# Optimization experiments

Hardware: AMD Instinct MI355X
Metric: run time of the kernel (lower is better)

The kernel has to match this reference:

```python
import jax, jax.numpy as jnp
import numpy as np

B, N, C = 8, 2000, 81
MAX_INST = 100
MIN_CONF = 0.7
NMS_THR = 0.3
BBOX_STD = jnp.array([0.1, 0.1, 0.2, 0.2], dtype=jnp.float32)
CLASS_OFFSET = 4.0  # per-class box offset so one NMS == per-class NMS


def setup_inputs() -> dict:
    key = jax.random.key(0)
    k1, k2, k3, k4 = jax.random.split(key, 4)
    # well-formed normalized rois: y1<y2, x1<x2
    ctr = jax.random.uniform(k1, (B, N, 2), minval=0.2, maxval=0.8)
    sz = jax.random.uniform(k2, (B, N, 2), minval=0.02, maxval=0.3)
    y1x1 = jnp.clip(ctr - 0.5 * sz, 0.0, 1.0)
    y2x2 = jnp.clip(ctr + 0.5 * sz, 0.0, 1.0)
    rois = jnp.concatenate([y1x1, y2x2], axis=-1).astype(jnp.float32)
    mrcnn_class = jax.nn.softmax(4.0 * jax.random.normal(k3, (B, N, C)), axis=-1).astype(jnp.float32)
    mrcnn_bbox = (0.1 * jax.random.normal(k4, (B, N, C, 4))).astype(jnp.float32)
    # meta: [image_id(1), orig_shape(3), image_shape(3), window(4), scale(1), active_class_ids(C)]
    meta_row = np.concatenate([
        np.array([0.0]), np.array([1024.0, 1024.0, 3.0]), np.array([1024.0, 1024.0, 3.0]),
        np.array([0.0, 0.0, 1024.0, 1024.0]), np.array([1.0]), np.ones(C)]).astype(np.float32)
    image_meta = jnp.broadcast_to(jnp.asarray(meta_row), (B, 12 + C))
    return {"rois": rois, "mrcnn_class": mrcnn_class, "mrcnn_bbox": mrcnn_bbox, "image_meta": image_meta}


def _apply_box_deltas(boxes, deltas):  # [N,4],[N,4]
    h = boxes[:, 2] - boxes[:, 0]
    w = boxes[:, 3] - boxes[:, 1]
    cy = boxes[:, 0] + 0.5 * h + deltas[:, 0] * h
    cx = boxes[:, 1] + 0.5 * w + deltas[:, 1] * w
    h = h * jnp.exp(deltas[:, 2])
    w = w * jnp.exp(deltas[:, 3])
    return jnp.stack([cy - 0.5 * h, cx - 0.5 * w, cy + 0.5 * h, cx + 0.5 * w], axis=1)


def _clip_boxes(boxes, window):  # window: [4]
    wy1, wx1, wy2, wx2 = window[0], window[1], window[2], window[3]
    y1 = jnp.clip(boxes[:, 0], wy1, wy2)
    x1 = jnp.clip(boxes[:, 1], wx1, wx2)
    y2 = jnp.clip(boxes[:, 2], wy1, wy2)
    x2 = jnp.clip(boxes[:, 3], wx1, wx2)
    return jnp.stack([y1, x1, y2, x2], axis=1)


def _pairwise_iou(b):  # [N,4] -> [N,N]
    area = (b[:, 2] - b[:, 0]) * (b[:, 3] - b[:, 1])
    iy = jnp.maximum(0.0, jnp.minimum(b[:, None, 2], b[None, :, 2]) - jnp.maximum(b[:, None, 0], b[None, :, 0]))
    ix = jnp.maximum(0.0, jnp.minimum(b[:, None, 3], b[None, :, 3]) - jnp.maximum(b[:, None, 1], b[None, :, 1]))
    inter = iy * ix
    return inter / (area[:, None] + area[None, :] - inter + 1e-12)


def _refine_one(rois, probs, deltas, window):
    n = rois.shape[0]
    class_ids = jnp.argmax(probs, axis=1)                      # [N]
    idx = jnp.arange(n)
    scores = probs[idx, class_ids]                              # [N]
    ds = deltas[idx, class_ids] * BBOX_STD                      # [N,4]
    refined = _clip_boxes(_apply_box_deltas(rois, ds), window)  # [N,4]
    valid = (class_ids > 0) & (scores >= MIN_CONF)
    # per-class NMS via class-offset trick (classes can never overlap)
    off_boxes = refined + CLASS_OFFSET * class_ids.astype(jnp.float32)[:, None]
    order = jnp.argsort(-jnp.where(valid, scores, -1.0))
    b_sorted = off_boxes[order]
    iou = _pairwise_iou(b_sorted)                               # [N,N]
    pos = jnp.arange(n)

    def body(keep, i):
        sup = keep[i] & (iou[i] > NMS_THR) & (pos > i)
        return keep & ~sup, None

    keep_sorted, _ = jax.lax.scan(body, valid[order], pos)
    keep = jnp.zeros(n, bool).at[order].set(keep_sorted)
    # per-class cap at MAX_INST (mirror max_output_size of per-class NMS)
    same = class_ids[:, None] == class_ids[None, :]
    before = (scores[None, :] > scores[:, None]) | ((scores[None, :] == scores[:, None]) & (pos[None, :] < pos[:, None]))
    rank = jnp.sum(keep[None, :] & same & before, axis=1)
    keep = keep & (rank < MAX_INST)
    # global top-k by score, pad with zeros
    masked = jnp.where(keep, scores, -1.0)
    top_scores, top_idx = jax.lax.top_k(masked, MAX_INST)
    valid_out = top_scores > 0.0
    det = jnp.concatenate([
        refined[top_idx],
        class_ids[top_idx].astype(jnp.float32)[:, None],
        scores[top_idx][:, None]], axis=1)                      # [MAX_INST,6]
    return jnp.where(valid_out[:, None], det, 0.0)


def reference(rois, mrcnn_class, mrcnn_bbox, image_meta):
    # normalize per-image window using image_shape of first image (as in original)
    image_shape = image_meta[0, 4:7]
    h, w = image_shape[0], image_shape[1]
    scale = jnp.stack([h, w, h, w]) - 1.0
    shift = jnp.array([0.0, 0.0, 1.0, 1.0], dtype=jnp.float32)
    window = (image_meta[:, 7:11] - shift) / scale              # [B,4]
    det = jax.vmap(_refine_one)(rois, mrcnn_class, mrcnn_bbox, window)
    return det.reshape(rois.shape[0], MAX_INST, 6)
```

## Files before the change

### kernel.cpp

```cpp
#include <hip/hip_runtime.h>
#include <stdint.h>

#define Bn 8
#define Nn 2000
#define Cc 81
#define META_STRIDE (12 + Cc)
#define MAXI 100
#define MINCONF 0.7f
#define NMSTHR 0.3f
#define PB_ROIS 128
#define PSTRIDE 83
#define SELT 320
#define SELCAP 512

__device__ __forceinline__ uint32_t ford(float f) {
    uint32_t u = __float_as_uint(f);
    return (u & 0x80000000u) ? ~u : (u | 0x80000000u);
}

__device__ __forceinline__ unsigned long long shflx64(unsigned long long v, int lx) {
    unsigned int lo = (unsigned int)v, hi = (unsigned int)(v >> 32);
    lo = (unsigned int)__shfl_xor((int)lo, lx, 64);
    hi = (unsigned int)__shfl_xor((int)hi, lx, 64);
    return ((unsigned long long)hi << 32) | lo;
}

__global__ void __launch_bounds__(256)
k_prep(const float* __restrict__ rois,
       const float* __restrict__ probs,
       const float* __restrict__ bbox,
       const float* __restrict__ meta,
       float* __restrict__ refined,
       float* __restrict__ score,
       int* __restrict__ cls,
       unsigned long long* __restrict__ keys) {
    __shared__ float sp[PB_ROIS * PSTRIDE];
    int tid  = threadIdx.x;
    int base = blockIdx.x * PB_ROIS;

    const float* gp = probs + (size_t)base * Cc;
    const int total = PB_ROIS * Cc;
    int r = tid / Cc, c = tid - r * Cc;
    for (int idx = tid; idx < total; idx += 256) {
        sp[r * PSTRIDE + c] = gp[idx];
        r += 3; c += 13;
        if (c >= Cc) { c -= Cc; r += 1; }
    }
    __syncthreads();

    int row  = tid >> 1;
    int half = tid & 1;
    const float* sr = sp + row * PSTRIDE;
    int   c0 = half ? 41 : 0;
    int   c1 = half ? Cc : 41;
    float v  = sr[c0];
    int   cb = c0;
    for (int cc2 = c0 + 1; cc2 < c1; ++cc2) {
        float x = sr[cc2];
        if (x > v) { v = x; cb = cc2; }
    }
    float vo = __shfl_xor(v, 1, 64);
    int   co = __shfl_xor(cb, 1, 64);
    float vA = half ? vo : v;   int cA = half ? co : cb;
    float vB = half ? v  : vo;  int cB = half ? cb : co;
    float sbest;  int cbest;
    if (vB > vA) { sbest = vB; cbest = cB; }
    else         { sbest = vA; cbest = cA; }

    if (half) return;
    int t = base + row;

    float4 d4 = reinterpret_cast<const float4*>(bbox)[(size_t)t * Cc + cbest];
    float dy = d4.x * 0.1f, dx = d4.y * 0.1f, dh = d4.z * 0.2f, dw = d4.w * 0.2f;

    float4 r4 = reinterpret_cast<const float4*>(rois)[t];
    float y1 = r4.x, x1 = r4.y, y2 = r4.z, x2 = r4.w;
    float h = y2 - y1, w = x2 - x1;
    float cy = y1 + 0.5f * h + dy * h;
    float cx = x1 + 0.5f * w + dx * w;
    h = h * expf(dh);
    w = w * expf(dw);
    float ny1 = cy - 0.5f * h, nx1 = cx - 0.5f * w;
    float ny2 = cy + 0.5f * h, nx2 = cx + 0.5f * w;

    int b = t / Nn;
    float sy = meta[4] - 1.0f, sx = meta[5] - 1.0f;
    const float* mb = meta + (size_t)b * META_STRIDE;
    float wy1 = mb[7] / sy;
    float wx1 = mb[8] / sx;
    float wy2 = (mb[9]  - 1.0f) / sy;
    float wx2 = (mb[10] - 1.0f) / sx;

    ny1 = fminf(fmaxf(ny1, wy1), wy2);
    nx1 = fminf(fmaxf(nx1, wx1), wx2);
    ny2 = fminf(fmaxf(ny2, wy1), wy2);
    nx2 = fminf(fmaxf(nx2, wx1), wx2);

    reinterpret_cast<float4*>(refined)[t] = float4{ny1, nx1, ny2, nx2};
    score[t] = sbest;
    cls[t]   = cbest;

    int i = t - b * Nn;
    bool valid = (cbest > 0) && (sbest >= MINCONF);
    float ks = valid ? sbest : -1.0f;
    keys[t] = ((unsigned long long)ford(ks) << 32) |
              (unsigned long long)(0xFFFFFFFFu - (uint32_t)i);
}

__global__ void __launch_bounds__(1024, 1)
k_nms(const unsigned long long* __restrict__ keys,
      const float* __restrict__ refined,
      const float* __restrict__ score,
      const int* __restrict__ cls,
      float* __restrict__ out) {
    __shared__ unsigned long long sk[SELCAP];
    __shared__ float4 sboxL[SELCAP];
    __shared__ int h1[256], h2[256], sc[257];
    __shared__ unsigned long long intraw[64];
    __shared__ unsigned long long extw[16];
    __shared__ int klist[128];
    __shared__ int sNk, sB, sSuf, sTheta, scnt;

    int b = blockIdx.x, tid = threadIdx.x;
    int wid = tid >> 6, lane = tid & 63;
    int e0 = tid << 1;

    const unsigned long long* kb = keys + (size_t)b * Nn;
    unsigned long long k0 = (e0     < Nn) ? kb[e0]     : 0ull;
    unsigned long long k1 = (e0 + 1 < Nn) ? kb[e0 + 1] : 0ull;

    if (tid < 256) { h1[tid] = 0; h2[tid] = 0; }
    if (tid < SELCAP) sk[tid] = 0ull;
    if (tid == 0) { sB = -2; sSuf = 0; sTheta = 0x8000; scnt = 0; sNk = 0; sc[256] = 0; }
    __syncthreads();

    if (k0 >> 63) atomicAdd(&h1[(int)(k0 >> 56) & 255], 1);
    if (k1 >> 63) atomicAdd(&h1[(int)(k1 >> 56) & 255], 1);
    __syncthreads();

    if (wid == 0) {
        int b0 = lane << 2;
        int v0 = h1[b0], v1 = h1[b0 + 1], v2 = h1[b0 + 2], v3 = h1[b0 + 3];
        int s3 = v3, s2 = v2 + s3, s1 = v1 + s2, s0 = v0 + s1;
        int G = s0;
        #pragma unroll
        for (int off = 1; off < 64; off <<= 1) {
            int u = __shfl_down(G, off, 64);
            if (lane + off < 64) G += u;
        }
        int A = G - s0;
        sc[b0] = A + s0; sc[b0 + 1] = A + s1; sc[b0 + 2] = A + s2; sc[b0 + 3] = A + s3;
    }
    __syncthreads();
    if (tid < 256) {
        int c = sc[tid], cn = sc[tid + 1];
        if (c >= SELT && cn < SELT) { sB = tid; sSuf = cn; }
    }
    __syncthreads();
    int B = sB;

    if (B >= 0) {
        if ((k0 >> 63) && (((int)(k0 >> 56) & 255) == B))
            atomicAdd(&h2[(int)(k0 >> 48) & 255], 1);
        if ((k1 >> 63) && (((int)(k1 >> 56) & 255) == B))
            atomicAdd(&h2[(int)(k1 >> 48) & 255], 1);
        __syncthreads();
        if (wid == 0) {
            int b0 = lane << 2;
            int v0 = h2[b0], v1 = h2[b0 + 1], v2 = h2[b0 + 2], v3 = h2[b0 + 3];
            int s3 = v3, s2 = v2 + s3, s1 = v1 + s2, s0 = v0 + s1;
            int G = s0;
            #pragma unroll
            for (int off = 1; off < 64; off <<= 1) {
                int u = __shfl_down(G, off, 64);
                if (lane + off < 64) G += u;
            }
            int A = G - s0;
            sc[b0] = A + s0; sc[b0 + 1] = A + s1; sc[b0 + 2] = A + s2; sc[b0 + 3] = A + s3;
        }
        __syncthreads();
        if (tid < 256) {
            int c  = sSuf + sc[tid];
            int cn = sSuf + sc[tid + 1];
            if (c >= SELT && cn < SELT) sTheta = (B << 8) | tid;
        }
    }
    __syncthreads();

    unsigned th = (unsigned)sTheta;
    if ((unsigned)(k0 >> 48) >= th) {
        int s = atomicAdd(&scnt, 1);
        if (s < SELCAP) sk[s] = k0;
    }
    if ((unsigned)(k1 >> 48) >= th) {
        int s = atomicAdd(&scnt, 1);
        if (s < SELCAP) sk[s] = k1;
    }
    __syncthreads();
    int S = scnt; if (S > SELCAP) S = SELCAP;

    if (tid < 256) {
        unsigned long long a = sk[e0], bv = sk[e0 + 1];
        for (int k = 2; k <= 128; k <<= 1) {
            bool desc = ((e0 & k) == 0);
            for (int j = k >> 1; j >= 2; j >>= 1) {
                int lx = j >> 1;
                bool keepmax = (desc == ((lane & lx) == 0));
                unsigned long long oa = shflx64(a, lx);
                unsigned long long ob = shflx64(bv, lx);
                a  = keepmax ? (a  > oa ? a  : oa) : (a  < oa ? a  : oa);
                bv = keepmax ? (bv > ob ? bv : ob) : (bv < ob ? bv : ob);
            }
            bool sw = desc ? (a < bv) : (a > bv);
            if (sw) { unsigned long long t2 = a; a = bv; bv = t2; }
        }
        sk[e0] = a; sk[e0 + 1] = bv;
    }
    __syncthreads();

    for (int k = 256; k <= SELCAP; k <<= 1) {
        for (int j = k >> 1; j >= 128; j >>= 1) {
            for (int t = tid; t < SELCAP; t += 1024) {
                int ixj = t ^ j;
                if (ixj > t) {
                    unsigned long long x = sk[t], y = sk[ixj];
                    bool desc = ((t & k) == 0);
                    if (desc ? (x < y) : (x > y)) { sk[t] = y; sk[ixj] = x; }
                }
            }
            __syncthreads();
        }
        if (tid < 256) {
            unsigned long long a = sk[e0], bv = sk[e0 + 1];
            bool desc = ((e0 & k) == 0);
            #pragma unroll
            for (int lx = 32; lx >= 1; lx >>= 1) {
                bool keepmax = (desc == ((lane & lx) == 0));
                unsigned long long oa = shflx64(a, lx);
                unsigned long long ob = shflx64(bv, lx);
                a  = keepmax ? (a  > oa ? a  : oa) : (a  < oa ? a  : oa);
                bv = keepmax ? (bv > ob ? bv : ob) : (bv < ob ? bv : ob);
            }
            bool sw = desc ? (a < bv) : (a > bv);
            if (sw) { unsigned long long t2 = a; a = bv; bv = t2; }
            sk[e0] = a; sk[e0 + 1] = bv;
        }
        __syncthreads();
    }

    for (int t = tid; t < S; t += 1024) {
        uint32_t oi = 0xFFFFFFFFu - (uint32_t)(sk[t] & 0xFFFFFFFFull);
        int gi = b * Nn + (int)oi;
        float off = 4.0f * (float)cls[gi];
        float4 rf = reinterpret_cast<const float4*>(refined)[gi];
        sboxL[t] = float4{rf.x + off, rf.y + off, rf.z + off, rf.w + off};
    }
    __syncthreads();

    int nblocks = (S + 63) >> 6;
    for (int t = 0; t < nblocks; ++t) {
        int base = t << 6;
        int nb = S - base; if (nb > 64) nb = 64;
        int K = sNk;

        float4 cb = (lane < nb) ? sboxL[base + lane] : float4{0.f, 0.f, 0.f, 0.f};
        float a2 = (cb.z - cb.x) * (cb.w - cb.y);

        bool supext = false;
        for (int k = wid; k < K; k += 16) {
            float4 kbx = sboxL[klist[k]];
            float ar = (kbx.z - kbx.x) * (kbx.w - kbx.y);
            float iy = fmaxf(0.0f, fminf(kbx.z, cb.z) - fmaxf(kbx.x, cb.x));
            float ix = fmaxf(0.0f, fminf(kbx.w, cb.w) - fmaxf(kbx.y, cb.y));
            float inter = iy * ix;
            float iou = inter / (ar + a2 - inter + 1e-12f);
            supext |= (lane < nb) && (iou > NMSTHR);
        }
        unsigned long long bw = __ballot(supext);
        if (lane == 0) extw[wid] = bw;

        #pragma unroll
        for (int s = 0; s < 4; ++s) {
            int rr = (wid << 2) + s;
            bool sup = false;
            if (rr < nb && lane < nb && lane > rr) {
                float4 rb = sboxL[base + rr];
                float ar = (rb.z - rb.x) * (rb.w - rb.y);
                float iy = fmaxf(0.0f, fminf(rb.z, cb.z) - fmaxf(rb.x, cb.x));
                float ix = fmaxf(0.0f, fminf(rb.w, cb.w) - fmaxf(rb.y, cb.y));
                float inter = iy * ix;
                float iou = inter / (ar + a2 - inter + 1e-12f);
                sup = iou > NMSTHR;
            }
            unsigned long long rb2 = __ballot(sup);
            if (lane == 0) intraw[rr] = rb2;
        }
        __syncthreads();

        if (wid == 0) {
            unsigned long long intra_l = intraw[lane];
            unsigned long long e = (lane < 16) ? extw[lane] : 0ull;
            #pragma unroll
            for (int m = 8; m >= 1; m >>= 1) e |= __shfl_xor(e, m, 64);
            e = __shfl(e, 0, 64);

            unsigned long long candm =
                (nb < 64 ? ((1ull << nb) - 1ull) : ~0ull) & ~e;
            int nk = K;
            while (candm) {
                int i = __builtin_ctzll(candm);
                if (lane == 0) klist[nk] = base + i;
                ++nk;
                if (nk >= MAXI) break;
                unsigned long long rowi = __shfl(intra_l, i, 64);
                candm &= ~rowi & ~((2ull << i) - 1ull);
            }
            if (lane == 0) sNk = nk;
        }
        __syncthreads();
        if (sNk >= MAXI) break;
    }

    int ne = sNk < MAXI ? sNk : MAXI;
    for (int r = tid; r < ne; r += 1024) {
        int pos = klist[r];
        uint32_t oi = 0xFFFFFFFFu - (uint32_t)(sk[pos] & 0xFFFFFFFFull);
        int gi = b * Nn + (int)oi;
        float4 rf = reinterpret_cast<const float4*>(refined)[gi];
        float* orow = out + ((size_t)b * MAXI + r) * 6;
        orow[0] = rf.x;
        orow[1] = rf.y;
        orow[2] = rf.z;
        orow[3] = rf.w;
        orow[4] = (float)cls[gi];
        orow[5] = score[gi];
    }
    for (int tt = ne * 6 + tid; tt < MAXI * 6; tt += 1024)
        out[(size_t)b * MAXI * 6 + tt] = 0.0f;
}

extern "C" void kernel_launch(void* const* d_in, const int* in_sizes, int n_in,
                              void* d_out, int out_size, void* d_ws, size_t ws_size,
                              hipStream_t stream) {
    const float* rois  = (const float*)d_in[0];
    const float* probs = (const float*)d_in[1];
    const float* bbox  = (const float*)d_in[2];
    const float* meta  = (const float*)d_in[3];
    float* out = (float*)d_out;

    const int BN = Bn * Nn;
    char* ws = (char*)d_ws;
    size_t off = 0;
    auto alloc = [&](size_t bytes) {
        void* p = ws + off;
        off += (bytes + 255) & ~(size_t)255;
        return p;
    };
    float*              refined = (float*)              alloc((size_t)BN * 4 * sizeof(float));
    float*              score   = (float*)              alloc((size_t)BN * sizeof(float));
    int*                cls     = (int*)                alloc((size_t)BN * sizeof(int));
    unsigned long long* keys    = (unsigned long long*) alloc((size_t)BN * sizeof(unsigned long long));
    (void)ws_size; (void)in_sizes; (void)n_in; (void)out_size;

    k_prep<<<BN / PB_ROIS, 256, 0, stream>>>(rois, probs, bbox, meta,
                                             refined, score, cls, keys);
    k_nms<<<Bn, 1024, 0, stream>>>(keys, refined, score, cls, out);
}
```

Measured before the change: 39.06 us.

## Shrink NMS block to 256 threads and use a single-pass histogram threshold

The NMS kernel now launches 256 threads instead of 1024, with each thread holding 8 keys in registers. Candidate selection builds one 256-bin histogram over the second key byte instead of a two-level radix select. That shortcut assumes every valid score shares the same top key byte, which holds for scores in [0.7, 1.0). Fewer waves make block barriers cheaper, but each wave does more suppression work against the kept list, and a score of exactly 1.0 would break the threshold assumption.

Result: slower. 43.09 us (+10.3%).

```diff
diff --git a/kernel.cpp b/kernel.cpp
--- a/kernel.cpp
+++ b/kernel.cpp
@@ -107,7 +107,7 @@
               (unsigned long long)(0xFFFFFFFFu - (uint32_t)i);
 }
 
-__global__ void __launch_bounds__(1024, 1)
+__global__ void __launch_bounds__(256, 1)
 k_nms(const unsigned long long* __restrict__ keys,
       const float* __restrict__ refined,
       const float* __restrict__ score,
@@ -115,32 +115,37 @@
       float* __restrict__ out) {
     __shared__ unsigned long long sk[SELCAP];
     __shared__ float4 sboxL[SELCAP];
-    __shared__ int h1[256], h2[256], sc[257];
+    __shared__ int h2[256], sc[257];
     __shared__ unsigned long long intraw[64];
-    __shared__ unsigned long long extw[16];
+    __shared__ unsigned long long extw[4];
     __shared__ int klist[128];
-    __shared__ int sNk, sB, sSuf, sTheta, scnt;
+    __shared__ int sNk, sTheta, scnt;
 
     int b = blockIdx.x, tid = threadIdx.x;
     int wid = tid >> 6, lane = tid & 63;
     int e0 = tid << 1;
 
     const unsigned long long* kb = keys + (size_t)b * Nn;
-    unsigned long long k0 = (e0     < Nn) ? kb[e0]     : 0ull;
-    unsigned long long k1 = (e0 + 1 < Nn) ? kb[e0 + 1] : 0ull;
-
-    if (tid < 256) { h1[tid] = 0; h2[tid] = 0; }
-    if (tid < SELCAP) sk[tid] = 0ull;
-    if (tid == 0) { sB = -2; sSuf = 0; sTheta = 0x8000; scnt = 0; sNk = 0; sc[256] = 0; }
-    __syncthreads();
-
-    if (k0 >> 63) atomicAdd(&h1[(int)(k0 >> 56) & 255], 1);
-    if (k1 >> 63) atomicAdd(&h1[(int)(k1 >> 56) & 255], 1);
+    unsigned long long kr[8];
+    #pragma unroll
+    for (int p = 0; p < 4; ++p) {
+        int e = (p << 9) + e0;
+        kr[2 * p]     = (e     < Nn) ? kb[e]     : 0ull;
+        kr[2 * p + 1] = (e + 1 < Nn) ? kb[e + 1] : 0ull;
+    }
+    h2[tid] = 0;
+    sk[tid] = 0ull; sk[tid + 256] = 0ull;
+    if (tid == 0) { sTheta = 0; scnt = 0; sNk = 0; sc[256] = 0; }
+    __syncthreads();
+
+    #pragma unroll
+    for (int p = 0; p < 8; ++p)
+        if (kr[p] >> 63) atomicAdd(&h2[(int)(kr[p] >> 48) & 255], 1);
     __syncthreads();
 
     if (wid == 0) {
         int b0 = lane << 2;
-        int v0 = h1[b0], v1 = h1[b0 + 1], v2 = h1[b0 + 2], v3 = h1[b0 + 3];
+        int v0 = h2[b0], v1 = h2[b0 + 1], v2 = h2[b0 + 2], v3 = h2[b0 + 3];
         int s3 = v3, s2 = v2 + s3, s1 = v1 + s2, s0 = v0 + s1;
         int G = s0;
         #pragma unroll
@@ -152,54 +157,25 @@
         sc[b0] = A + s0; sc[b0 + 1] = A + s1; sc[b0 + 2] = A + s2; sc[b0 + 3] = A + s3;
     }
     __syncthreads();
-    if (tid < 256) {
+    {
         int c = sc[tid], cn = sc[tid + 1];
-        if (c >= SELT && cn < SELT) { sB = tid; sSuf = cn; }
-    }
-    __syncthreads();
-    int B = sB;
-
-    if (B >= 0) {
-        if ((k0 >> 63) && (((int)(k0 >> 56) & 255) == B))
-            atomicAdd(&h2[(int)(k0 >> 48) & 255], 1);
-        if ((k1 >> 63) && (((int)(k1 >> 56) & 255) == B))
-            atomicAdd(&h2[(int)(k1 >> 48) & 255], 1);
-        __syncthreads();
-        if (wid == 0) {
-            int b0 = lane << 2;
-            int v0 = h2[b0], v1 = h2[b0 + 1], v2 = h2[b0 + 2], v3 = h2[b0 + 3];
-            int s3 = v3, s2 = v2 + s3, s1 = v1 + s2, s0 = v0 + s1;
-            int G = s0;
-            #pragma unroll
-            for (int off = 1; off < 64; off <<= 1) {
-                int u = __shfl_down(G, off, 64);
-                if (lane + off < 64) G += u;
-            }
-            int A = G - s0;
-            sc[b0] = A + s0; sc[b0 + 1] = A + s1; sc[b0 + 2] = A + s2; sc[b0 + 3] = A + s3;
-        }
-        __syncthreads();
-        if (tid < 256) {
-            int c  = sSuf + sc[tid];
-            int cn = sSuf + sc[tid + 1];
-            if (c >= SELT && cn < SELT) sTheta = (B << 8) | tid;
-        }
+        if (c >= SELT && cn < SELT) sTheta = tid;
     }
     __syncthreads();
 
     unsigned th = (unsigned)sTheta;
-    if ((unsigned)(k0 >> 48) >= th) {
-        int s = atomicAdd(&scnt, 1);
-        if (s < SELCAP) sk[s] = k0;
-    }
-    if ((unsigned)(k1 >> 48) >= th) {
-        int s = atomicAdd(&scnt, 1);
-        if (s < SELCAP) sk[s] = k1;
+    #pragma unroll
+    for (int p = 0; p < 8; ++p) {
+        unsigned long long k = kr[p];
+        if ((k >> 63) && (((unsigned)(k >> 48) & 255u) >= th)) {
+            int s = atomicAdd(&scnt, 1);
+            if (s < SELCAP) sk[s] = k;
+        }
     }
     __syncthreads();
     int S = scnt; if (S > SELCAP) S = SELCAP;
 
-    if (tid < 256) {
+    {
         unsigned long long a = sk[e0], bv = sk[e0 + 1];
         for (int k = 2; k <= 128; k <<= 1) {
             bool desc = ((e0 & k) == 0);
@@ -220,7 +196,9 @@
 
     for (int k = 256; k <= SELCAP; k <<= 1) {
         for (int j = k >> 1; j >= 128; j >>= 1) {
-            for (int t = tid; t < SELCAP; t += 1024) {
+            #pragma unroll
+            for (int rep = 0; rep < 2; ++rep) {
+                int t = tid + (rep << 8);
                 int ixj = t ^ j;
                 if (ixj > t) {
                     unsigned long long x = sk[t], y = sk[ixj];
@@ -230,7 +208,7 @@
             }
             __syncthreads();
         }
-        if (tid < 256) {
+        {
             unsigned long long a = sk[e0], bv = sk[e0 + 1];
             bool desc = ((e0 & k) == 0);
             #pragma unroll
@@ -248,7 +226,7 @@
         __syncthreads();
     }
 
-    for (int t = tid; t < S; t += 1024) {
+    for (int t = tid; t < S; t += 256) {
         uint32_t oi = 0xFFFFFFFFu - (uint32_t)(sk[t] & 0xFFFFFFFFull);
         int gi = b * Nn + (int)oi;
         float off = 4.0f * (float)cls[gi];
@@ -267,7 +245,7 @@
         float a2 = (cb.z - cb.x) * (cb.w - cb.y);
 
         bool supext = false;
-        for (int k = wid; k < K; k += 16) {
+        for (int k = wid; k < K; k += 4) {
             float4 kbx = sboxL[klist[k]];
             float ar = (kbx.z - kbx.x) * (kbx.w - kbx.y);
             float iy = fmaxf(0.0f, fminf(kbx.z, cb.z) - fmaxf(kbx.x, cb.x));
@@ -280,8 +258,8 @@
         if (lane == 0) extw[wid] = bw;
 
         #pragma unroll
-        for (int s = 0; s < 4; ++s) {
-            int rr = (wid << 2) + s;
+        for (int s = 0; s < 16; ++s) {
+            int rr = (wid << 4) + s;
             bool sup = false;
             if (rr < nb && lane < nb && lane > rr) {
                 float4 rb = sboxL[base + rr];
@@ -299,9 +277,9 @@
 
         if (wid == 0) {
             unsigned long long intra_l = intraw[lane];
-            unsigned long long e = (lane < 16) ? extw[lane] : 0ull;
-            #pragma unroll
-            for (int m = 8; m >= 1; m >>= 1) e |= __shfl_xor(e, m, 64);
+            unsigned long long e = (lane < 4) ? extw[lane] : 0ull;
+            e |= shflx64(e, 2);
+            e |= shflx64(e, 1);
             e = __shfl(e, 0, 64);
 
             unsigned long long candm =
@@ -322,7 +300,7 @@
     }
 
     int ne = sNk < MAXI ? sNk : MAXI;
-    for (int r = tid; r < ne; r += 1024) {
+    for (int r = tid; r < ne; r += 256) {
         int pos = klist[r];
         uint32_t oi = 0xFFFFFFFFu - (uint32_t)(sk[pos] & 0xFFFFFFFFull);
         int gi = b * Nn + (int)oi;
@@ -335,7 +313,7 @@
         orow[4] = (float)cls[gi];
         orow[5] = score[gi];
     }
-    for (int tt = ne * 6 + tid; tt < MAXI * 6; tt += 1024)
+    for (int tt = ne * 6 + tid; tt < MAXI * 6; tt += 256)
         out[(size_t)b * MAXI * 6 + tt] = 0.0f;
 }
 
@@ -364,5 +342,5 @@
 
     k_prep<<<BN / PB_ROIS, 256, 0, stream>>>(rois, probs, bbox, meta,
                                              refined, score, cls, keys);
-    k_nms<<<Bn, 1024, 0, stream>>>(keys, refined, score, cls, out);
-}
+    k_nms<<<Bn, 256, 0, stream>>>(keys, refined, score, cls, out);
+}
```
